# Kernel tuning notes

Hardware: AMD Instinct MI355X
Metric: run time of the kernel (lower is better)

## Reference

```python
import jax, jax.numpy as jnp
import numpy as np


def setup_inputs() -> dict:
    key = jax.random.key(0)
    k1, k2 = jax.random.split(key)
    z = jax.random.normal(k1, (16, 1024, 512), dtype=jnp.float32)
    codebook = jax.random.normal(k2, (2048, 64), dtype=jnp.float32)
    return {"z": z, "codebook": codebook}


def reference(z, codebook):
    """VQQuantizer.forward: group latent, euclidean nearest-codebook quantize,
    straight-through estimator, commit loss = mse(stop_grad(z_q), z).
    Returns (codes, indices, commit_loss) matching dict values
    {'codes','indices','commit_loss'} ('z' and 'state' are z_grouped / codes).
    """
    D = codebook.shape[1]            # codebook_dim
    shp = z.shape                    # [B, T, latent]
    zg = z.reshape(shp[:-1] + (-1, D))   # [B, T, G, D]
    zf = zg.reshape(-1, D)               # [N, D], N = B*T*G
    # squared euclidean distances: ||z||^2 - 2 z.c + ||c||^2  -> [N, K]
    dist = (
        jnp.sum(zf * zf, axis=1, keepdims=True)
        - 2.0 * (zf @ codebook.T)
        + jnp.sum(codebook * codebook, axis=1)
    )
    idx = jnp.argmin(dist, axis=-1)      # [N]
    zq = codebook[idx].reshape(zg.shape)  # [B, T, G, D]
    commit_loss = jnp.mean((jax.lax.stop_gradient(zq) - zg) ** 2)
    # straight-through
    zq_st = zg + jax.lax.stop_gradient(zq - zg)
    codes = zq_st.reshape(shp)            # [B, T, latent]
    indices = idx.reshape(zg.shape[:-1])  # [B, T, G]
    return codes, indices, commit_loss
```

## Files before the change

### kernel.cpp

```cpp
#include <hip/hip_runtime.h>

typedef short s16x8 __attribute__((ext_vector_type(8)));
typedef float f32x4 __attribute__((ext_vector_type(4)));

#define CODES_ELEMS 8388608
#define N_ROWS      131072
#define IDX_OFF     CODES_ELEMS
#define LOSS_OFF    (CODES_ELEMS + N_ROWS)

#define WS_LOSS 0
#define WS_CNT  4
#define WS_CC   64
#define WS_CBS  8448
#define WS_LIST 532736
#define MARGIN_T 0.05f

__device__ __forceinline__ float bf2f(unsigned short h) { return __uint_as_float(((unsigned)h) << 16); }
__device__ __forceinline__ unsigned short f2bf(float f) {
  unsigned u = __float_as_uint(f);
  u += 0x7fffu + ((u >> 16) & 1u);
  return (unsigned short)(u >> 16);
}
__device__ __forceinline__ void gl_lds16(const void* g, void* l) {
  __builtin_amdgcn_global_load_lds(
      (__attribute__((address_space(1))) void*)(g),
      (__attribute__((address_space(3))) void*)(l), 16, 0, 0);
}

__global__ __launch_bounds__(256) void vq_prep1(const float* __restrict__ cb,
                                                float* __restrict__ cc,
                                                float* __restrict__ loss,
                                                int* __restrict__ cnt) {
  int t = threadIdx.x;
  if (blockIdx.x == 0 && t == 0) { loss[0] = 0.f; cnt[0] = 0; }
  int e = blockIdx.x * 256 + t;
  float v = cb[e];
  float s = v * v;
  #pragma unroll
  for (int m = 1; m < 64; m <<= 1) s += __shfl_xor(s, m, 64);
  if ((t & 63) == 0) cc[e >> 6] = s;
}

__global__ __launch_bounds__(256) void vq_prep2(const float* __restrict__ cb,
                                                unsigned short* __restrict__ cbs) {
  int e = blockIdx.x * 256 + threadIdx.x;
  int k = e >> 7, K = e & 127;
  int s = K >> 5, rem = K & 31, q = rem >> 3, j = rem & 7;
  int d = (s < 2) ? K : (K - 64);
  float c = cb[k * 64 + d];
  unsigned short c1 = f2bf(c);
  unsigned short val = (s < 2) ? c1 : f2bf(c - bf2f(c1));
  int chunk = k >> 7, ct = (k >> 4) & 7, n = k & 15;
  cbs[(((chunk * 4 + s) * 8 + ct) * 64 + (q * 16 + n)) * 8 + j] = val;
}

__global__ __launch_bounds__(256) void VQQuantizer_30064771072206_kernel(
    const float* __restrict__ zf, const unsigned short* __restrict__ cbs,
    const float* __restrict__ cc, int* __restrict__ cnt, int* __restrict__ list,
    float* __restrict__ out)
{
  __shared__ __align__(16) unsigned short bt[24576];
  __shared__ float cc_l[128];
  const int t = threadIdx.x, w = t >> 6, l = t & 63;
  const int col = l & 15, q = l >> 4;
  const int R0 = blockIdx.x * 128;
  const float4* zf4 = (const float4*)zf;

  s16x8 az1[2][2], az2[2][2];
  #pragma unroll
  for (int tile = 0; tile < 2; ++tile) {
    int row = R0 + tile * 64 + 16 * w + col;
    const float4* zr = zf4 + (size_t)row * 16;
    #pragma unroll
    for (int s = 0; s < 2; ++s) {
      float4 u0 = zr[s * 8 + q * 2];
      float4 u1 = zr[s * 8 + q * 2 + 1];
      float m2[8] = {-2.f*u0.x, -2.f*u0.y, -2.f*u0.z, -2.f*u0.w,
                     -2.f*u1.x, -2.f*u1.y, -2.f*u1.z, -2.f*u1.w};
      #pragma unroll
      for (int j = 0; j < 8; ++j) {
        unsigned short h1 = f2bf(m2[j]);
        unsigned short h2 = f2bf(m2[j] - bf2f(h1));
        az1[tile][s][j] = (short)h1;
        az2[tile][s][j] = (short)h2;
      }
    }
  }

  float v1[2][4], v2[2][4]; int i1[2][4];
  #pragma unroll
  for (int tile = 0; tile < 2; ++tile)
    #pragma unroll
    for (int r = 0; r < 4; ++r) {
      v1[tile][r] = 3.402823466e38f; v2[tile][r] = 3.402823466e38f; i1[tile][r] = 0;
    }

  for (int chunk = 0; chunk < 16; ++chunk) {
    if (chunk) __syncthreads();
    #pragma unroll
    for (int i = 0; i < 12; ++i) {
      int f = i * 256 + t;
      int s = f >> 9, ct_ = (f >> 6) & 7;
      int src_s = (s >= 4) ? s - 4 : s;
      gl_lds16(cbs + (size_t)chunk * 16384 + (size_t)((src_s * 8 + ct_) * 64 + l) * 8,
               &bt[(size_t)((s * 8 + ct_) * 64) * 8]);
    }
    if (t < 128) cc_l[t] = cc[chunk * 128 + t];
    __syncthreads();

    #pragma unroll
    for (int ct = 0; ct < 8; ++ct) {
      float nh = cc_l[ct * 16 + col];
      const unsigned short* base = &bt[(ct * 64 + l) * 8];
      s16x8 b0 = *(const s16x8*)(base + 0 * 4096);
      s16x8 b1 = *(const s16x8*)(base + 1 * 4096);
      s16x8 b2 = *(const s16x8*)(base + 2 * 4096);
      s16x8 b3 = *(const s16x8*)(base + 3 * 4096);
      s16x8 b4 = *(const s16x8*)(base + 4 * 4096);
      s16x8 b5 = *(const s16x8*)(base + 5 * 4096);
      int code = chunk * 128 + ct * 16 + col;
      #pragma unroll
      for (int tile = 0; tile < 2; ++tile) {
        f32x4 acc; acc[0] = nh; acc[1] = nh; acc[2] = nh; acc[3] = nh;
        acc = __builtin_amdgcn_mfma_f32_16x16x32_bf16(az1[tile][0], b0, acc, 0, 0, 0);
        acc = __builtin_amdgcn_mfma_f32_16x16x32_bf16(az1[tile][1], b1, acc, 0, 0, 0);
        acc = __builtin_amdgcn_mfma_f32_16x16x32_bf16(az1[tile][0], b2, acc, 0, 0, 0);
        acc = __builtin_amdgcn_mfma_f32_16x16x32_bf16(az1[tile][1], b3, acc, 0, 0, 0);
        acc = __builtin_amdgcn_mfma_f32_16x16x32_bf16(az2[tile][0], b4, acc, 0, 0, 0);
        acc = __builtin_amdgcn_mfma_f32_16x16x32_bf16(az2[tile][1], b5, acc, 0, 0, 0);
        #pragma unroll
        for (int r = 0; r < 4; ++r) {
          float d = acc[r];
          bool lt = d < v1[tile][r];
          v2[tile][r] = lt ? v1[tile][r] : fminf(v2[tile][r], d);
          i1[tile][r] = lt ? code : i1[tile][r];
          v1[tile][r] = lt ? d : v1[tile][r];
        }
      }
    }
  }

  #pragma unroll
  for (int tile = 0; tile < 2; ++tile) {
    #pragma unroll
    for (int r = 0; r < 4; ++r) {
      float a = v1[tile][r], b2v = v2[tile][r]; int ia = i1[tile][r];
      #pragma unroll
      for (int m = 1; m < 16; m <<= 1) {
        float oa = __shfl_xor(a, m, 64);
        int   oi = __shfl_xor(ia, m, 64);
        float ob = __shfl_xor(b2v, m, 64);
        float hi = fmaxf(a, oa);
        b2v = fminf(fminf(b2v, ob), hi);
        bool take = (oa < a) || (oa == a && oi < ia);
        a = take ? oa : a; ia = take ? oi : ia;
      }
      v1[tile][r] = a; v2[tile][r] = b2v; i1[tile][r] = ia;
    }
    if (col == 0) {
      #pragma unroll
      for (int r = 0; r < 4; ++r) {
        int row = R0 + tile * 64 + 16 * w + q * 4 + r;
        out[IDX_OFF + row] = (float)i1[tile][r];
        if (v2[tile][r] - v1[tile][r] < MARGIN_T) {
          int p = atomicAdd(cnt, 1);
          list[p] = row;
        }
      }
    }
  }
}

__global__ __launch_bounds__(256) void vq_rescore(
    const float* __restrict__ zf, const float* __restrict__ cb,
    const float* __restrict__ cc, const int* __restrict__ cnt,
    const int* __restrict__ list, float* __restrict__ out)
{
  __shared__ __align__(16) float zl[8][68];
  __shared__ float zz_l[8];
  __shared__ int   rows_s[8];
  __shared__ float rv[4][8];
  __shared__ int   ri[4][8];
  const int t = threadIdx.x, w = t >> 6, l = t & 63;
  const int count = cnt[0];
  const float4* cb4 = (const float4*)cb;

  for (int itb = blockIdx.x; itb * 8 < count; itb += 1024) {
    if (itb != (int)blockIdx.x) __syncthreads();
    if (t < 8) {
      int ii = itb * 8 + t;
      rows_s[t] = list[ii < count ? ii : count - 1];
    }
    __syncthreads();
    if (t < 128) {
      int r = t >> 4, dq = t & 15;
      *(float4*)&zl[r][dq * 4] = ((const float4*)zf)[(size_t)rows_s[r] * 16 + dq];
    }
    __syncthreads();
    if (t < 8) {
      float s = 0.f;
      for (int d = 0; d < 64; ++d) { float v = zl[t][d]; s += v * v; }
      zz_l[t] = s;
    }
    __syncthreads();

    float bv[8]; int bi[8];
    #pragma unroll
    for (int r = 0; r < 8; ++r) { bv[r] = 3.402823466e38f; bi[r] = 0; }
    #pragma unroll 1
    for (int o = 0; o < 8; ++o) {
      int c = o * 256 + t;
      const float4* cr = cb4 + (size_t)c * 16;
      float a[8];
      #pragma unroll
      for (int r = 0; r < 8; ++r) a[r] = 0.f;
      #pragma unroll
      for (int dq = 0; dq < 16; ++dq) {
        float4 cv = cr[dq];
        #pragma unroll
        for (int r = 0; r < 8; ++r) {
          float4 z4 = *(const float4*)&zl[r][dq * 4];
          a[r] += z4.x * cv.x;
          a[r] += z4.y * cv.y;
          a[r] += z4.z * cv.z;
          a[r] += z4.w * cv.w;
        }
      }
      float ccv = cc[c];
      #pragma unroll
      for (int r = 0; r < 8; ++r) {
        float t0 = zz_l[r] - 2.0f * a[r];
        float dist = t0 + ccv;
        if (dist < bv[r]) { bv[r] = dist; bi[r] = c; }
      }
    }
    #pragma unroll
    for (int r = 0; r < 8; ++r) {
      float v = bv[r]; int idx = bi[r];
      #pragma unroll
      for (int m = 1; m < 64; m <<= 1) {
        float ov = __shfl_xor(v, m, 64); int oi = __shfl_xor(idx, m, 64);
        if (ov < v || (ov == v && oi < idx)) { v = ov; idx = oi; }
      }
      if (l == 0) { rv[w][r] = v; ri[w][r] = idx; }
    }
    __syncthreads();
    if (t < 8) {
      float fv = rv[0][t]; int fi = ri[0][t];
      #pragma unroll
      for (int k = 1; k < 4; ++k) {
        if (rv[k][t] < fv || (rv[k][t] == fv && ri[k][t] < fi)) { fv = rv[k][t]; fi = ri[k][t]; }
      }
      out[IDX_OFF + rows_s[t]] = (float)fi;
    }
  }
}

__global__ __launch_bounds__(256) void vq_epilogue(
    const float* __restrict__ zf, const float* __restrict__ cb,
    float* __restrict__ loss, float* __restrict__ out)
{
  __shared__ int idxb[64];
  __shared__ float wsum[4];
  int t = threadIdx.x;
  int R0 = blockIdx.x * 64;
  if (t < 64) idxb[t] = (int)out[IDX_OFF + R0 + t];
  __syncthreads();
  const float4* zf4 = (const float4*)zf;
  const float4* cb4 = (const float4*)cb;
  float4* out4 = (float4*)out;
  float lsum = 0.f;
  #pragma unroll
  for (int i = 0; i < 4; ++i) {
    int f = i * 256 + t;
    int row = f >> 4, dq = f & 15;
    int k = idxb[row];
    float4 qv = cb4[(size_t)k * 16 + dq];
    float4 zv = zf4[(size_t)(R0 + row) * 16 + dq];
    float dx = qv.x - zv.x, dy = qv.y - zv.y, dz = qv.z - zv.z, dw = qv.w - zv.w;
    float4 st; st.x = zv.x + dx; st.y = zv.y + dy; st.z = zv.z + dz; st.w = zv.w + dw;
    out4[(size_t)(R0 + row) * 16 + dq] = st;
    lsum += dx * dx; lsum += dy * dy; lsum += dz * dz; lsum += dw * dw;
  }
  #pragma unroll
  for (int m = 1; m < 64; m <<= 1) lsum += __shfl_xor(lsum, m, 64);
  if ((t & 63) == 0) wsum[t >> 6] = lsum;
  __syncthreads();
  if (t == 0) atomicAdd(loss, wsum[0] + wsum[1] + wsum[2] + wsum[3]);
}

__global__ void vq_finalize(const float* __restrict__ loss, float* __restrict__ out) {
  out[LOSS_OFF] = loss[0] * (1.f / 8388608.f);
}

extern "C" void kernel_launch(void* const* d_in, const int* in_sizes, int n_in,
                              void* d_out, int out_size, void* d_ws, size_t ws_size,
                              hipStream_t stream) {
  const float* z  = (const float*)d_in[0];
  const float* cb = (const float*)d_in[1];
  float* out = (float*)d_out;
  float* loss = (float*)((char*)d_ws + WS_LOSS);
  int*   cnt  = (int*)((char*)d_ws + WS_CNT);
  float* cc   = (float*)((char*)d_ws + WS_CC);
  unsigned short* cbs = (unsigned short*)((char*)d_ws + WS_CBS);
  int*   list = (int*)((char*)d_ws + WS_LIST);

  vq_prep1<<<512, 256, 0, stream>>>(cb, cc, loss, cnt);
  vq_prep2<<<1024, 256, 0, stream>>>(cb, cbs);
  VQQuantizer_30064771072206_kernel<<<1024, 256, 0, stream>>>(z, cbs, cc, cnt, list, out);
  vq_rescore<<<1024, 256, 0, stream>>>(z, cb, cc, cnt, list, out);
  vq_epilogue<<<2048, 256, 0, stream>>>(z, cb, loss, out);
  vq_finalize<<<1, 1, 0, stream>>>(loss, out);
}
```

Baseline: 294.2 us.

## Double-buffer codebook chunks, pack index into distance bits, merge prep kernels

Merges the two codebook prep kernels into one. The main kernel now handles 256 rows per block with four tiles and double-buffers the codebook chunk in LDS, so the next chunk's load overlaps compute. It also stops duplicating the high-bf16 codebook slabs in LDS and loads all norms up front. The argmin bookkeeping packs a chunk/ct id into the low mantissa bits of the distance, leaving integer min/max work per element, and the row norm is added so packed values stay positive. The loss of mantissa precision is covered by a wider rescore margin, at the cost of more rows sent to rescoring.

```diff
diff --git a/kernel.cpp b/kernel.cpp
--- a/kernel.cpp
+++ b/kernel.cpp
@@ -13,7 +13,7 @@
 #define WS_CC   64
 #define WS_CBS  8448
 #define WS_LIST 532736
-#define MARGIN_T 0.05f
+#define MARGIN_T 0.0625f
 
 __device__ __forceinline__ float bf2f(unsigned short h) { return __uint_as_float(((unsigned)h) << 16); }
 __device__ __forceinline__ unsigned short f2bf(float f) {
@@ -27,23 +27,14 @@
       (__attribute__((address_space(3))) void*)(l), 16, 0, 0);
 }
 
-__global__ __launch_bounds__(256) void vq_prep1(const float* __restrict__ cb,
-                                                float* __restrict__ cc,
-                                                float* __restrict__ loss,
-                                                int* __restrict__ cnt) {
+__global__ __launch_bounds__(256) void vq_prep(const float* __restrict__ cb,
+                                               float* __restrict__ cc,
+                                               unsigned short* __restrict__ cbs,
+                                               float* __restrict__ loss,
+                                               int* __restrict__ cnt) {
   int t = threadIdx.x;
   if (blockIdx.x == 0 && t == 0) { loss[0] = 0.f; cnt[0] = 0; }
   int e = blockIdx.x * 256 + t;
-  float v = cb[e];
-  float s = v * v;
-  #pragma unroll
-  for (int m = 1; m < 64; m <<= 1) s += __shfl_xor(s, m, 64);
-  if ((t & 63) == 0) cc[e >> 6] = s;
-}
-
-__global__ __launch_bounds__(256) void vq_prep2(const float* __restrict__ cb,
-                                                unsigned short* __restrict__ cbs) {
-  int e = blockIdx.x * 256 + threadIdx.x;
   int k = e >> 7, K = e & 127;
   int s = K >> 5, rem = K & 31, q = rem >> 3, j = rem & 7;
   int d = (s < 2) ? K : (K - 64);
@@ -52,6 +43,10 @@
   unsigned short val = (s < 2) ? c1 : f2bf(c - bf2f(c1));
   int chunk = k >> 7, ct = (k >> 4) & 7, n = k & 15;
   cbs[(((chunk * 4 + s) * 8 + ct) * 64 + (q * 16 + n)) * 8 + j] = val;
+  float sq = c * c;
+  #pragma unroll
+  for (int m = 1; m < 64; m <<= 1) sq += __shfl_xor(sq, m, 64);
+  if ((t & 63) == 0) cc[k] = sq;
 }
 
 __global__ __launch_bounds__(256) void VQQuantizer_30064771072206_kernel(
@@ -59,22 +54,37 @@
     const float* __restrict__ cc, int* __restrict__ cnt, int* __restrict__ list,
     float* __restrict__ out)
 {
-  __shared__ __align__(16) unsigned short bt[24576];
-  __shared__ float cc_l[128];
+  __shared__ __align__(16) unsigned short bt[2][16384];
+  __shared__ __align__(16) float cc_l[2048];
   const int t = threadIdx.x, w = t >> 6, l = t & 63;
   const int col = l & 15, q = l >> 4;
-  const int R0 = blockIdx.x * 128;
+  const int R0 = blockIdx.x * 256;
   const float4* zf4 = (const float4*)zf;
 
-  s16x8 az1[2][2], az2[2][2];
-  #pragma unroll
-  for (int tile = 0; tile < 2; ++tile) {
+  #pragma unroll
+  for (int i = 0; i < 8; ++i) {
+    int unit = i * 4 + w;
+    gl_lds16(cbs + (size_t)(unit * 64 + l) * 8, &bt[0][unit * 512]);
+  }
+  #pragma unroll
+  for (int i = 0; i < 2; ++i) {
+    int idx = i * 256 + t;
+    ((float4*)cc_l)[idx] = ((const float4*)cc)[idx];
+  }
+
+  s16x8 az1[4][2], az2[4][2];
+  float zzr[4][4];
+  #pragma unroll
+  for (int tile = 0; tile < 4; ++tile) {
     int row = R0 + tile * 64 + 16 * w + col;
     const float4* zr = zf4 + (size_t)row * 16;
+    float zzp = 0.f;
     #pragma unroll
     for (int s = 0; s < 2; ++s) {
       float4 u0 = zr[s * 8 + q * 2];
       float4 u1 = zr[s * 8 + q * 2 + 1];
+      zzp += u0.x*u0.x + u0.y*u0.y + u0.z*u0.z + u0.w*u0.w;
+      zzp += u1.x*u1.x + u1.y*u1.y + u1.z*u1.z + u1.w*u1.w;
       float m2[8] = {-2.f*u0.x, -2.f*u0.y, -2.f*u0.z, -2.f*u0.w,
                      -2.f*u1.x, -2.f*u1.y, -2.f*u1.z, -2.f*u1.w};
       #pragma unroll
@@ -85,66 +95,76 @@
         az2[tile][s][j] = (short)h2;
       }
     }
-  }
-
-  float v1[2][4], v2[2][4]; int i1[2][4];
-  #pragma unroll
-  for (int tile = 0; tile < 2; ++tile)
-    #pragma unroll
-    for (int r = 0; r < 4; ++r) {
-      v1[tile][r] = 3.402823466e38f; v2[tile][r] = 3.402823466e38f; i1[tile][r] = 0;
-    }
-
+    zzp += __shfl_xor(zzp, 16, 64);
+    zzp += __shfl_xor(zzp, 32, 64);
+    #pragma unroll
+    for (int r = 0; r < 4; ++r)
+      zzr[tile][r] = __shfl(zzp, q * 4 + r, 64);
+  }
+
+  unsigned p1[4][4], p2[4][4];
+  #pragma unroll
+  for (int tile = 0; tile < 4; ++tile)
+    #pragma unroll
+    for (int r = 0; r < 4; ++r) { p1[tile][r] = 0xFFFFFFFFu; p2[tile][r] = 0xFFFFFFFFu; }
+
+  __syncthreads();
+
+  int cur = 0;
   for (int chunk = 0; chunk < 16; ++chunk) {
-    if (chunk) __syncthreads();
-    #pragma unroll
-    for (int i = 0; i < 12; ++i) {
-      int f = i * 256 + t;
-      int s = f >> 9, ct_ = (f >> 6) & 7;
-      int src_s = (s >= 4) ? s - 4 : s;
-      gl_lds16(cbs + (size_t)chunk * 16384 + (size_t)((src_s * 8 + ct_) * 64 + l) * 8,
-               &bt[(size_t)((s * 8 + ct_) * 64) * 8]);
-    }
-    if (t < 128) cc_l[t] = cc[chunk * 128 + t];
-    __syncthreads();
-
+    if (chunk + 1 < 16) {
+      const unsigned short* src = cbs + (size_t)(chunk + 1) * 16384;
+      unsigned short* dst = &bt[cur ^ 1][0];
+      #pragma unroll
+      for (int i = 0; i < 8; ++i) {
+        int unit = i * 4 + w;
+        gl_lds16(src + (size_t)(unit * 64 + l) * 8, dst + unit * 512);
+      }
+    }
+    const unsigned short* bb = &bt[cur][l * 8];
+    const float* ccc = &cc_l[chunk * 128 + col];
     #pragma unroll
     for (int ct = 0; ct < 8; ++ct) {
-      float nh = cc_l[ct * 16 + col];
-      const unsigned short* base = &bt[(ct * 64 + l) * 8];
-      s16x8 b0 = *(const s16x8*)(base + 0 * 4096);
-      s16x8 b1 = *(const s16x8*)(base + 1 * 4096);
-      s16x8 b2 = *(const s16x8*)(base + 2 * 4096);
-      s16x8 b3 = *(const s16x8*)(base + 3 * 4096);
-      s16x8 b4 = *(const s16x8*)(base + 4 * 4096);
-      s16x8 b5 = *(const s16x8*)(base + 5 * 4096);
-      int code = chunk * 128 + ct * 16 + col;
-      #pragma unroll
-      for (int tile = 0; tile < 2; ++tile) {
-        f32x4 acc; acc[0] = nh; acc[1] = nh; acc[2] = nh; acc[3] = nh;
+      float nh = ccc[ct * 16];
+      const unsigned short* base = bb + ct * 512;
+      s16x8 b0 = *(const s16x8*)(base);
+      s16x8 b1 = *(const s16x8*)(base + 4096);
+      s16x8 b2 = *(const s16x8*)(base + 8192);
+      s16x8 b3 = *(const s16x8*)(base + 12288);
+      unsigned pid = (unsigned)(chunk * 8 + ct);
+      #pragma unroll
+      for (int tile = 0; tile < 4; ++tile) {
+        f32x4 acc;
+        acc[0] = nh + zzr[tile][0];
+        acc[1] = nh + zzr[tile][1];
+        acc[2] = nh + zzr[tile][2];
+        acc[3] = nh + zzr[tile][3];
         acc = __builtin_amdgcn_mfma_f32_16x16x32_bf16(az1[tile][0], b0, acc, 0, 0, 0);
         acc = __builtin_amdgcn_mfma_f32_16x16x32_bf16(az1[tile][1], b1, acc, 0, 0, 0);
         acc = __builtin_amdgcn_mfma_f32_16x16x32_bf16(az1[tile][0], b2, acc, 0, 0, 0);
         acc = __builtin_amdgcn_mfma_f32_16x16x32_bf16(az1[tile][1], b3, acc, 0, 0, 0);
-        acc = __builtin_amdgcn_mfma_f32_16x16x32_bf16(az2[tile][0], b4, acc, 0, 0, 0);
-        acc = __builtin_amdgcn_mfma_f32_16x16x32_bf16(az2[tile][1], b5, acc, 0, 0, 0);
+        acc = __builtin_amdgcn_mfma_f32_16x16x32_bf16(az2[tile][0], b0, acc, 0, 0, 0);
+        acc = __builtin_amdgcn_mfma_f32_16x16x32_bf16(az2[tile][1], b1, acc, 0, 0, 0);
         #pragma unroll
         for (int r = 0; r < 4; ++r) {
-          float d = acc[r];
-          bool lt = d < v1[tile][r];
-          v2[tile][r] = lt ? v1[tile][r] : fminf(v2[tile][r], d);
-          i1[tile][r] = lt ? code : i1[tile][r];
-          v1[tile][r] = lt ? d : v1[tile][r];
+          unsigned pd = (__float_as_uint(acc[r]) & 0xFFFFFF80u) | pid;
+          unsigned mx = p1[tile][r] > pd ? p1[tile][r] : pd;
+          p2[tile][r] = p2[tile][r] < mx ? p2[tile][r] : mx;
+          p1[tile][r] = p1[tile][r] < pd ? p1[tile][r] : pd;
         }
       }
     }
-  }
-
-  #pragma unroll
-  for (int tile = 0; tile < 2; ++tile) {
+    __syncthreads();
+    cur ^= 1;
+  }
+
+  #pragma unroll
+  for (int tile = 0; tile < 4; ++tile) {
     #pragma unroll
     for (int r = 0; r < 4; ++r) {
-      float a = v1[tile][r], b2v = v2[tile][r]; int ia = i1[tile][r];
+      float a   = __uint_as_float(p1[tile][r] & 0xFFFFFF80u);
+      int   ia  = (int)(p1[tile][r] & 127u) * 16 + col;
+      float b2v = __uint_as_float(p2[tile][r] & 0xFFFFFF80u);
       #pragma unroll
       for (int m = 1; m < 16; m <<= 1) {
         float oa = __shfl_xor(a, m, 64);
@@ -155,14 +175,10 @@
         bool take = (oa < a) || (oa == a && oi < ia);
         a = take ? oa : a; ia = take ? oi : ia;
       }
-      v1[tile][r] = a; v2[tile][r] = b2v; i1[tile][r] = ia;
-    }
-    if (col == 0) {
-      #pragma unroll
-      for (int r = 0; r < 4; ++r) {
+      if (col == 0) {
         int row = R0 + tile * 64 + 16 * w + q * 4 + r;
-        out[IDX_OFF + row] = (float)i1[tile][r];
-        if (v2[tile][r] - v1[tile][r] < MARGIN_T) {
+        out[IDX_OFF + row] = (float)ia;
+        if (b2v - a < MARGIN_T) {
           int p = atomicAdd(cnt, 1);
           list[p] = row;
         }
@@ -305,9 +321,8 @@
   unsigned short* cbs = (unsigned short*)((char*)d_ws + WS_CBS);
   int*   list = (int*)((char*)d_ws + WS_LIST);
 
-  vq_prep1<<<512, 256, 0, stream>>>(cb, cc, loss, cnt);
-  vq_prep2<<<1024, 256, 0, stream>>>(cb, cbs);
-  VQQuantizer_30064771072206_kernel<<<1024, 256, 0, stream>>>(z, cbs, cc, cnt, list, out);
+  vq_prep<<<1024, 256, 0, stream>>>(cb, cc, cbs, loss, cnt);
+  VQQuantizer_30064771072206_kernel<<<512, 256, 0, stream>>>(z, cbs, cc, cnt, list, out);
   vq_rescore<<<1024, 256, 0, stream>>>(z, cb, cc, cnt, list, out);
   vq_epilogue<<<2048, 256, 0, stream>>>(z, cb, loss, out);
   vq_finalize<<<1, 1, 0, stream>>>(loss, out);
```

Measured after the change: 282.6 us. 1.04x faster.
